# Kernel tuning notes

Measured on AMD Instinct MI355X. Metric: run time of the kernel, lower is better.

Reference implementation:

```python
import jax, jax.numpy as jnp
import numpy as np

N, H, TAU = 320, 160, 257
EPS = 1e-5
LAG_CUT = 33  # output keeps lags 33..TAU-1


def setup_inputs() -> dict:
    key = jax.random.key(0)
    x = jax.random.normal(key, (32, 160000), dtype=jnp.float32)
    return {"x": x}


def reference(x):
    B, S = x.shape
    # prepare_input: pad with H zeros, frame with unfold(N, H)
    xp = jnp.concatenate([x, jnp.zeros((B, H), x.dtype)], axis=1)
    Fn = (S + H - N) // H + 1  # num_frames (static)
    idx = jnp.arange(Fn)[:, None] * H + jnp.arange(N)[None, :]
    frames = xp[:, idx]                      # (B, Fn, N)

    # extract: torch rolls the FLATTENED frames tensor (B, Fn*N) by -tau.
    # x_tau frame f is the window xf[f*N + tau : f*N + tau + N] (circular over Fn*N).
    xf = frames.reshape(B, Fn * N)
    ext_full = jnp.concatenate([xf, xf[:, :TAU - 1]], axis=1)  # circular wrap
    widx = jnp.arange(Fn)[:, None] * N + jnp.arange(N + TAU - 1)[None, :]
    ext = ext_full[:, widx]                  # (B, Fn, N+TAU-1)

    # numerator for all lags at once via grouped 1D cross-correlation
    inp = ext.reshape(1, B * Fn, N + TAU - 1)   # NCW
    ker = frames.reshape(B * Fn, 1, N)          # OIW
    num = jax.lax.conv_general_dilated(
        inp, ker, window_strides=(1,), padding='VALID',
        feature_group_count=B * Fn)             # (1, B*Fn, TAU)
    num = num.reshape(B, Fn, TAU)

    # energies: sum(x*x) per frame, and sliding sum(x_tau*x_tau) via cumsum
    e0 = jnp.sum(frames * frames, axis=-1)      # (B, Fn)
    cs = jnp.concatenate(
        [jnp.zeros((B, Fn, 1), x.dtype), jnp.cumsum(ext * ext, axis=-1)], axis=-1)
    e_tau = cs[..., N:N + TAU] - cs[..., :TAU]  # (B, Fn, TAU)

    xcorr = 2.0 * num / (e0[..., None] + e_tau + EPS)
    return xcorr[:, :, LAG_CUT:]
```

## Files before the change

kernel.cpp:

```cpp
#include <hip/hip_runtime.h>


typedef _Float16 f16;
typedef _Float16 h8 __attribute__((ext_vector_type(8)));
typedef _Float16 h4 __attribute__((ext_vector_type(4)));
typedef float    f4 __attribute__((ext_vector_type(4)));

#define S_LEN 160000
#define FN    1000
#define NF    8
#define BLOCK 256
#define USZ   1536

#define ZPAD_OFF 0
#define SE_OFF   16
#define SO_OFF   3152
#define TH_OFF   6288
#define TO_OFF   6864
#define BRE_OFF  7440
#define BRO_OFF  7952
#define CSG_OFF  8464
#define CST_OFF  14672
#define TOT_OFF  15712
#define SMEM_SZ  16752

__global__ __launch_bounds__(BLOCK)
void xcorr_kernel(const float* __restrict__ x, float* __restrict__ out) {
    __shared__ __align__(16) unsigned char smem[SMEM_SZ];
    f16*      zpad = (f16*)(smem + ZPAD_OFF);
    f16*      s_h  = (f16*)(smem + SE_OFF);
    unsigned* sOd  = (unsigned*)(smem + SO_OFF);
    f16*      T_h  = (f16*)(smem + TH_OFF);
    unsigned* TOd  = (unsigned*)(smem + TO_OFF);
    f16*      brE  = (f16*)(smem + BRE_OFF);
    unsigned* brOd = (unsigned*)(smem + BRO_OFF);
    float*    csg  = (float*)(smem + CSG_OFF);
    float*    csT  = (float*)(smem + CST_OFF);
    float*    tot  = (float*)(smem + TOT_OFF);

    const int tid   = threadIdx.x;
    const int b     = blockIdx.y;
    const int fbase = blockIdx.x * NF;
    const long bOff = (long)b * S_LEN;
    const int gbase = fbase * 160;
    const bool lastBlk = (fbase + NF >= FN);

    for (int i = 4*tid; i < USZ; i += 4*BLOCK) {
        const int gx = gbase + i;
        float v0, v1, v2, v3;
        if (gx + 3 < S_LEN) {
            const float4 v = *(const float4*)&x[bOff + gx];
            v0 = v.x; v1 = v.y; v2 = v.z; v3 = v.w;
        } else {
            v0 = (gx+0 < S_LEN) ? x[bOff+gx+0] : 0.f;
            v1 = (gx+1 < S_LEN) ? x[bOff+gx+1] : 0.f;
            v2 = (gx+2 < S_LEN) ? x[bOff+gx+2] : 0.f;
            v3 = (gx+3 < S_LEN) ? x[bOff+gx+3] : 0.f;
        }
        h4 hv; hv[0]=(f16)v0; hv[1]=(f16)v1; hv[2]=(f16)v2; hv[3]=(f16)v3;
        *(h4*)&s_h[i] = hv;
        f4 sq; sq[0]=v0*v0; sq[1]=v1*v1; sq[2]=v2*v2; sq[3]=v3*v3;
        *(f4*)&csg[i] = sq;
    }
    if (tid < 8) {
        h4 z; z[0]=(f16)0.f; z[1]=(f16)0.f; z[2]=(f16)0.f; z[3]=(f16)0.f;
        *(h4*)&s_h[1536 + 4*tid] = z;
    }
    if (tid < 16) csg[1536 + tid] = 0.f;
    if (tid == 0) { uint4 z; z.x=z.y=z.z=z.w=0u; *(uint4*)(smem + ZPAD_OFF) = z; }
    if (lastBlk) {
        for (int j = tid; j < 288; j += BLOCK) {
            const float tv = (j < 256) ? x[bOff + j] : 0.f;
            T_h[j] = (f16)tv;
            if (j < 260) csT[j] = tv * tv;
        }
    }
    __syncthreads();

    {
        const unsigned* sEd = (const unsigned*)s_h;
        for (int idx = tid; idx < 196; idx += BLOCK) {
            uint4 lo4;
            if (idx) lo4 = *(const uint4*)(sEd + 4*idx - 4);
            else     { lo4.x=lo4.y=lo4.z=0u; lo4.w=0u; }
            const uint4 hi4 = *(const uint4*)(sEd + 4*idx);
            uint4 o;
            o.x = __builtin_amdgcn_alignbit(hi4.x, lo4.w, 16);
            o.y = __builtin_amdgcn_alignbit(hi4.y, hi4.x, 16);
            o.z = __builtin_amdgcn_alignbit(hi4.z, hi4.y, 16);
            o.w = __builtin_amdgcn_alignbit(hi4.w, hi4.z, 16);
            *(uint4*)(sOd + 4*idx) = o;
        }
        if (lastBlk) {
            const unsigned* THd = (const unsigned*)T_h;
            for (int idx = tid; idx < 36; idx += BLOCK) {
                uint4 lo4;
                if (idx) lo4 = *(const uint4*)(THd + 4*idx - 4);
                else     { lo4.x=lo4.y=lo4.z=0u; lo4.w=0u; }
                const uint4 hi4 = *(const uint4*)(THd + 4*idx);
                uint4 o;
                o.x = __builtin_amdgcn_alignbit(hi4.x, lo4.w, 16);
                o.y = __builtin_amdgcn_alignbit(hi4.y, hi4.x, 16);
                o.z = __builtin_amdgcn_alignbit(hi4.z, hi4.y, 16);
                o.w = __builtin_amdgcn_alignbit(hi4.w, hi4.z, 16);
                *(uint4*)(TOd + 4*idx) = o;
            }
        }
        {
            const int fi = tid >> 5, j = tid & 31;
            const int t = 304 + j;
            const bool lastF = lastBlk && (fbase + fi == FN-1);
            f16 v;
            if (t < 320)      v = s_h[160*fi + t];
            else if (lastF)   v = T_h[t - 320];
            else              v = s_h[160*fi + t - 160];
            brE[32*fi + j] = v;
        }
        if (tid < NF*16) {
            const int fi = tid >> 4, j = tid & 15;
            const int tl = 303 + 2*j, th = 304 + 2*j;
            const bool lastF = lastBlk && (fbase + fi == FN-1);
            const f16 lo = (tl < 320) ? s_h[160*fi + tl]
                          : (lastF ? T_h[tl-320] : s_h[160*fi + tl - 160]);
            const f16 hi = (th < 320) ? s_h[160*fi + th]
                          : (lastF ? T_h[th-320] : s_h[160*fi + th - 160]);
            union { struct { f16 a, c; } h; unsigned u; } pk;
            pk.h.a = lo; pk.h.c = hi;
            brOd[16*fi + j] = pk.u;
        }
    }
    float p[7]; float mytot = 0.f;
    {
        const int t0 = 7*tid;
#pragma unroll
        for (int e = 0; e < 7; ++e) {
            const float r = (t0+e < 1552) ? csg[t0+e] : 0.f;
            p[e] = mytot;
            mytot += r;
        }
        tot[tid] = mytot;
    }
    __syncthreads();

    const int lane = tid & 63;
    const int wv   = tid >> 6;
    {
        const float v = tot[tid];
        float sc = v;
#pragma unroll
        for (int d = 1; d < 64; d <<= 1) {
            const float o = __shfl_up(sc, d);
            sc += (lane >= d) ? o : 0.f;
        }
        tot[tid] = sc - v;
        if (lane == 63) tot[256 + wv] = sc;
        if (lastBlk && wv == 0) {
            float r[5]; float mt = 0.f;
#pragma unroll
            for (int e = 0; e < 5; ++e) {
                const int j = 5*lane + e;
                const float rv = (j < 260) ? csT[j] : 0.f;
                r[e] = mt; mt += rv;
            }
            float sc2 = mt;
#pragma unroll
            for (int d = 1; d < 64; d <<= 1) {
                const float o = __shfl_up(sc2, d);
                sc2 += (lane >= d) ? o : 0.f;
            }
            const float b2 = sc2 - mt;
#pragma unroll
            for (int e = 0; e < 5; ++e) {
                const int j = 5*lane + e;
                if (j < 260) csT[j] = b2 + r[e];
            }
        }
    }
    __syncthreads();

    {
        const float w1 = tot[256], w2 = tot[257], w3 = tot[258];
        const float wbase = ((wv > 0) ? w1 : 0.f) + ((wv > 1) ? w2 : 0.f)
                          + ((wv > 2) ? w3 : 0.f);
        const float base = wbase + tot[tid];
        const int t0 = 7*tid;
#pragma unroll
        for (int e = 0; e < 7; ++e)
            if (t0+e < 1552) csg[t0+e] = base + p[e];
    }
    __syncthreads();

    const int col  = lane & 15;
    const int q    = lane >> 4;
    const int off0 = 8*q - 16*col;
    const int tb0  = 33 + col + 8*q;
    const int pc   = tb0 & 1;
    const unsigned* bbS = pc ? sOd : (const unsigned*)s_h;
    const unsigned* bbT = pc ? TOd : (const unsigned*)T_h;

#pragma unroll 1
    for (int ff = 0; ff < 2; ++ff) {
        const int fi = 2*wv + ff;
        const int f  = fbase + fi;
        const bool isLast = (f == FN-1);
        const f16* frame = s_h + 160*fi;
        const int i0 = (160*fi + tb0 + pc) >> 1;
        const unsigned* pA = bbS + i0;
        const unsigned* pB = isLast ? (bbT + ((tb0 - 320 + pc) >> 1))
                                    : (bbS + (i0 - 80));
        const unsigned* brB = pc ? (brOd + 16*fi) : ((const unsigned*)brE + 16*fi);
        const unsigned* p8 = (tb0 <= 56) ? pA
                           : ((tb0 <= 63) ? (brB + ((tb0 - 48 + pc) >> 1) - 128)
                                          : pB);
        f4 acc = {0.f, 0.f, 0.f, 0.f};
#pragma unroll
        for (int s = 0; s < 17; ++s) {
            const int off = off0 + 32*s;
            const f16* ap = ((unsigned)off <= 312u) ? (frame + off) : zpad;
            const h8 a = *(const h8*)ap;
            const unsigned* bp = (s < 8) ? pA : ((s == 8) ? p8 : pB);
            union { unsigned u[4]; h8 h; } Bf;
            Bf.u[0] = bp[16*s + 0];
            Bf.u[1] = bp[16*s + 1];
            Bf.u[2] = bp[16*s + 2];
            Bf.u[3] = bp[16*s + 3];
            acc = __builtin_amdgcn_mfma_f32_16x16x32_f16(a, Bf.h, acc, 0, 0, 0);
        }
        const int D = 160*fi;
        const float c0   = csg[D];
        const float c160 = csg[D+160];
        const float c320 = csg[D+320];
        const float e0   = c320 - c0;
        float* op = &out[(long)(b*FN + f) * 224];
#pragma unroll
        for (int v = 0; v < 4; ++v) {
            const int t1 = 4*q + v;
            if (t1 <= 13) {
                const int tau = 33 + 16*t1 + col;
                const float et = isLast
                    ? (c320 - csg[D+tau] + csT[tau])
                    : (c320 - csg[D+tau] - c160 + csg[D+160+tau]);
                const float den = e0 + et + 1e-5f;
                op[tau - 33] = 2.f * acc[v] * __builtin_amdgcn_rcpf(den);
            }
        }
    }
}

extern "C" void kernel_launch(void* const* d_in, const int* in_sizes, int n_in,
                              void* d_out, int out_size, void* d_ws, size_t ws_size,
                              hipStream_t stream) {
    const float* x = (const float*)d_in[0];
    float* out = (float*)d_out;
    dim3 grid(FN / NF, 32);
    dim3 block(BLOCK);
    hipLaunchKernelGGL(xcorr_kernel, grid, block, 0, stream, x, out);
}
```

Measured before the change: 91.00 us.

## Use one wave per frame with 512 threads and prebuilt padded A-operand buffers

```diff
diff --git a/kernel.cpp b/kernel.cpp
--- a/kernel.cpp
+++ b/kernel.cpp
@@ -9,34 +9,35 @@
 #define S_LEN 160000
 #define FN    1000
 #define NF    8
-#define BLOCK 256
+#define BLOCK 512
 #define USZ   1536
 
-#define ZPAD_OFF 0
-#define SE_OFF   16
-#define SO_OFF   3152
-#define TH_OFF   6288
-#define TO_OFF   6864
-#define BRE_OFF  7440
-#define BRO_OFF  7952
-#define CSG_OFF  8464
-#define CST_OFF  14672
-#define TOT_OFF  15712
-#define SMEM_SZ  16752
+#define SH_OFF   0
+#define SO_OFF   3136
+#define TH_OFF   6272
+#define TO_OFF   6848
+#define BRO_OFF  7424
+#define FP0_OFF  7936
+#define FP1_OFF  13824
+#define CSG_OFF  19712
+#define CST_OFF  27904
+#define TOT_OFF  28944
+#define SMEM_SZ  31024
 
 __global__ __launch_bounds__(BLOCK)
 void xcorr_kernel(const float* __restrict__ x, float* __restrict__ out) {
     __shared__ __align__(16) unsigned char smem[SMEM_SZ];
-    f16*      zpad = (f16*)(smem + ZPAD_OFF);
-    f16*      s_h  = (f16*)(smem + SE_OFF);
+    f16*      s_h  = (f16*)(smem + SH_OFF);
     unsigned* sOd  = (unsigned*)(smem + SO_OFF);
     f16*      T_h  = (f16*)(smem + TH_OFF);
     unsigned* TOd  = (unsigned*)(smem + TO_OFF);
-    f16*      brE  = (f16*)(smem + BRE_OFF);
     unsigned* brOd = (unsigned*)(smem + BRO_OFF);
+    unsigned* fp0  = (unsigned*)(smem + FP0_OFF);
+    unsigned* fp1  = (unsigned*)(smem + FP1_OFF);
     float*    csg  = (float*)(smem + CSG_OFF);
     float*    csT  = (float*)(smem + CST_OFF);
     float*    tot  = (float*)(smem + TOT_OFF);
+    f4*       csg4 = (f4*)csg;
 
     const int tid   = threadIdx.x;
     const int b     = blockIdx.y;
@@ -45,45 +46,47 @@
     const int gbase = fbase * 160;
     const bool lastBlk = (fbase + NF >= FN);
 
-    for (int i = 4*tid; i < USZ; i += 4*BLOCK) {
-        const int gx = gbase + i;
-        float v0, v1, v2, v3;
-        if (gx + 3 < S_LEN) {
-            const float4 v = *(const float4*)&x[bOff + gx];
-            v0 = v.x; v1 = v.y; v2 = v.z; v3 = v.w;
+    {
+        const int i = 4 * tid;
+        if (i < USZ) {
+            const int gx = gbase + i;
+            float v0, v1, v2, v3;
+            if (gx + 3 < S_LEN) {
+                const float4 v = *(const float4*)&x[bOff + gx];
+                v0 = v.x; v1 = v.y; v2 = v.z; v3 = v.w;
+            } else {
+                v0 = (gx+0 < S_LEN) ? x[bOff+gx+0] : 0.f;
+                v1 = (gx+1 < S_LEN) ? x[bOff+gx+1] : 0.f;
+                v2 = (gx+2 < S_LEN) ? x[bOff+gx+2] : 0.f;
+                v3 = (gx+3 < S_LEN) ? x[bOff+gx+3] : 0.f;
+            }
+            h4 hv; hv[0]=(f16)v0; hv[1]=(f16)v1; hv[2]=(f16)v2; hv[3]=(f16)v3;
+            *(h4*)&s_h[i] = hv;
+            f4 sq; sq[0]=v0*v0; sq[1]=v1*v1; sq[2]=v2*v2; sq[3]=v3*v3;
+            csg4[tid] = sq;
         } else {
-            v0 = (gx+0 < S_LEN) ? x[bOff+gx+0] : 0.f;
-            v1 = (gx+1 < S_LEN) ? x[bOff+gx+1] : 0.f;
-            v2 = (gx+2 < S_LEN) ? x[bOff+gx+2] : 0.f;
-            v3 = (gx+3 < S_LEN) ? x[bOff+gx+3] : 0.f;
-        }
-        h4 hv; hv[0]=(f16)v0; hv[1]=(f16)v1; hv[2]=(f16)v2; hv[3]=(f16)v3;
-        *(h4*)&s_h[i] = hv;
-        f4 sq; sq[0]=v0*v0; sq[1]=v1*v1; sq[2]=v2*v2; sq[3]=v3*v3;
-        *(f4*)&csg[i] = sq;
+            f4 z; z[0]=z[1]=z[2]=z[3]=0.f;
+            csg4[tid] = z;
+        }
     }
     if (tid < 8) {
         h4 z; z[0]=(f16)0.f; z[1]=(f16)0.f; z[2]=(f16)0.f; z[3]=(f16)0.f;
         *(h4*)&s_h[1536 + 4*tid] = z;
     }
-    if (tid < 16) csg[1536 + tid] = 0.f;
-    if (tid == 0) { uint4 z; z.x=z.y=z.z=z.w=0u; *(uint4*)(smem + ZPAD_OFF) = z; }
-    if (lastBlk) {
-        for (int j = tid; j < 288; j += BLOCK) {
-            const float tv = (j < 256) ? x[bOff + j] : 0.f;
-            T_h[j] = (f16)tv;
-            if (j < 260) csT[j] = tv * tv;
-        }
-    }
-    __syncthreads();
-
-    {
-        const unsigned* sEd = (const unsigned*)s_h;
+    if (lastBlk && tid < 288) {
+        const float tv = (tid < 256) ? x[bOff + tid] : 0.f;
+        T_h[tid] = (f16)tv;
+        if (tid < 260) csT[tid] = tv * tv;
+    }
+    __syncthreads();
+
+    {
+        const unsigned* sd = (const unsigned*)s_h;
         for (int idx = tid; idx < 196; idx += BLOCK) {
             uint4 lo4;
-            if (idx) lo4 = *(const uint4*)(sEd + 4*idx - 4);
+            if (idx) lo4 = *(const uint4*)(sd + 4*idx - 4);
             else     { lo4.x=lo4.y=lo4.z=0u; lo4.w=0u; }
-            const uint4 hi4 = *(const uint4*)(sEd + 4*idx);
+            const uint4 hi4 = *(const uint4*)(sd + 4*idx);
             uint4 o;
             o.x = __builtin_amdgcn_alignbit(hi4.x, lo4.w, 16);
             o.y = __builtin_amdgcn_alignbit(hi4.y, hi4.x, 16);
@@ -92,12 +95,12 @@
             *(uint4*)(sOd + 4*idx) = o;
         }
         if (lastBlk) {
-            const unsigned* THd = (const unsigned*)T_h;
+            const unsigned* Td = (const unsigned*)T_h;
             for (int idx = tid; idx < 36; idx += BLOCK) {
                 uint4 lo4;
-                if (idx) lo4 = *(const uint4*)(THd + 4*idx - 4);
+                if (idx) lo4 = *(const uint4*)(Td + 4*idx - 4);
                 else     { lo4.x=lo4.y=lo4.z=0u; lo4.w=0u; }
-                const uint4 hi4 = *(const uint4*)(THd + 4*idx);
+                const uint4 hi4 = *(const uint4*)(Td + 4*idx);
                 uint4 o;
                 o.x = __builtin_amdgcn_alignbit(hi4.x, lo4.w, 16);
                 o.y = __builtin_amdgcn_alignbit(hi4.y, hi4.x, 16);
@@ -106,20 +109,34 @@
                 *(uint4*)(TOd + 4*idx) = o;
             }
         }
-        {
-            const int fi = tid >> 5, j = tid & 31;
-            const int t = 304 + j;
+        const uint4* sh4 = (const uint4*)s_h;
+        for (int idx = tid; idx < 368; idx += BLOCK) {
+            const int fi = idx / 46;
+            const int c  = idx - 46*fi;
+            uint4 o0, o1;
+            if (c < 2 || c > 42) {
+                o0.x=o0.y=o0.z=0u; o0.w=0u; o1 = o0;
+            } else if (c == 42) {
+                o0.x=o0.y=o0.z=0u; o0.w=0u;
+                const unsigned prev = sd[80*fi + 159];
+                o1.x = __builtin_amdgcn_alignbit(0u, prev, 16);
+                o1.y = 0u; o1.z = 0u; o1.w = 0u;
+            } else {
+                const uint4 A = sh4[20*fi + c - 2];
+                o0 = A;
+                const unsigned prev = (c == 2) ? 0u : sd[80*fi + 4*c - 9];
+                o1.x = __builtin_amdgcn_alignbit(A.x, prev, 16);
+                o1.y = __builtin_amdgcn_alignbit(A.y, A.x, 16);
+                o1.z = __builtin_amdgcn_alignbit(A.z, A.y, 16);
+                o1.w = __builtin_amdgcn_alignbit(A.w, A.z, 16);
+            }
+            *(uint4*)(fp0 + 184*fi + 4*c) = o0;
+            *(uint4*)(fp1 + 184*fi + 4*c) = o1;
+        }
+        if (tid < 128) {
+            const int fi = tid >> 4, j = tid & 15;
             const bool lastF = lastBlk && (fbase + fi == FN-1);
-            f16 v;
-            if (t < 320)      v = s_h[160*fi + t];
-            else if (lastF)   v = T_h[t - 320];
-            else              v = s_h[160*fi + t - 160];
-            brE[32*fi + j] = v;
-        }
-        if (tid < NF*16) {
-            const int fi = tid >> 4, j = tid & 15;
             const int tl = 303 + 2*j, th = 304 + 2*j;
-            const bool lastF = lastBlk && (fbase + fi == FN-1);
             const f16 lo = (tl < 320) ? s_h[160*fi + tl]
                           : (lastF ? T_h[tl-320] : s_h[160*fi + tl - 160]);
             const f16 hi = (th < 320) ? s_h[160*fi + th]
@@ -129,15 +146,14 @@
             brOd[16*fi + j] = pk.u;
         }
     }
-    float p[7]; float mytot = 0.f;
-    {
-        const int t0 = 7*tid;
-#pragma unroll
-        for (int e = 0; e < 7; ++e) {
-            const float r = (t0+e < 1552) ? csg[t0+e] : 0.f;
-            p[e] = mytot;
-            mytot += r;
-        }
+    float p[4]; float mytot;
+    {
+        const f4 v = csg4[tid];
+        p[0] = 0.f;
+        p[1] = v[0];
+        p[2] = v[0] + v[1];
+        p[3] = p[2] + v[2];
+        mytot = p[3] + v[3];
         tot[tid] = mytot;
     }
     __syncthreads();
@@ -153,7 +169,7 @@
             sc += (lane >= d) ? o : 0.f;
         }
         tot[tid] = sc - v;
-        if (lane == 63) tot[256 + wv] = sc;
+        if (lane == 63) tot[512 + wv] = sc;
         if (lastBlk && wv == 0) {
             float r[5]; float mt = 0.f;
 #pragma unroll
@@ -179,53 +195,48 @@
     __syncthreads();
 
     {
-        const float w1 = tot[256], w2 = tot[257], w3 = tot[258];
-        const float wbase = ((wv > 0) ? w1 : 0.f) + ((wv > 1) ? w2 : 0.f)
-                          + ((wv > 2) ? w3 : 0.f);
+        float wbase = 0.f;
+#pragma unroll
+        for (int w2 = 0; w2 < 7; ++w2)
+            wbase += (wv > w2) ? tot[512 + w2] : 0.f;
         const float base = wbase + tot[tid];
-        const int t0 = 7*tid;
-#pragma unroll
-        for (int e = 0; e < 7; ++e)
-            if (t0+e < 1552) csg[t0+e] = base + p[e];
-    }
-    __syncthreads();
-
-    const int col  = lane & 15;
-    const int q    = lane >> 4;
-    const int off0 = 8*q - 16*col;
-    const int tb0  = 33 + col + 8*q;
-    const int pc   = tb0 & 1;
-    const unsigned* bbS = pc ? sOd : (const unsigned*)s_h;
-    const unsigned* bbT = pc ? TOd : (const unsigned*)T_h;
-
-#pragma unroll 1
-    for (int ff = 0; ff < 2; ++ff) {
-        const int fi = 2*wv + ff;
-        const int f  = fbase + fi;
-        const bool isLast = (f == FN-1);
-        const f16* frame = s_h + 160*fi;
-        const int i0 = (160*fi + tb0 + pc) >> 1;
-        const unsigned* pA = bbS + i0;
-        const unsigned* pB = isLast ? (bbT + ((tb0 - 320 + pc) >> 1))
-                                    : (bbS + (i0 - 80));
-        const unsigned* brB = pc ? (brOd + 16*fi) : ((const unsigned*)brE + 16*fi);
-        const unsigned* p8 = (tb0 <= 56) ? pA
-                           : ((tb0 <= 63) ? (brB + ((tb0 - 48 + pc) >> 1) - 128)
-                                          : pB);
-        f4 acc = {0.f, 0.f, 0.f, 0.f};
-#pragma unroll
-        for (int s = 0; s < 17; ++s) {
-            const int off = off0 + 32*s;
-            const f16* ap = ((unsigned)off <= 312u) ? (frame + off) : zpad;
-            const h8 a = *(const h8*)ap;
-            const unsigned* bp = (s < 8) ? pA : ((s == 8) ? p8 : pB);
-            union { unsigned u[4]; h8 h; } Bf;
-            Bf.u[0] = bp[16*s + 0];
-            Bf.u[1] = bp[16*s + 1];
-            Bf.u[2] = bp[16*s + 2];
-            Bf.u[3] = bp[16*s + 3];
-            acc = __builtin_amdgcn_mfma_f32_16x16x32_f16(a, Bf.h, acc, 0, 0, 0);
-        }
+        f4 o; o[0]=base+p[0]; o[1]=base+p[1]; o[2]=base+p[2]; o[3]=base+p[3];
+        csg4[tid] = o;
+    }
+    __syncthreads();
+
+    const int col = lane & 15;
+    const int q   = lane >> 4;
+    const int fi  = wv;
+    const int f   = fbase + fi;
+    const bool isLast = (f == FN-1);
+
+    const unsigned* ap = (col & 1)
+        ? (fp1 + 184*fi + ((8*q - col + 17) >> 1))
+        : (fp0 + 184*fi + ((8*q - col + 16) >> 1));
+    const int tb0 = 33 + 14*col + 8*q;
+    const int j0  = (tb0 + 1) >> 1;
+    const unsigned* pA  = sOd + 80*fi + j0;
+    const unsigned* pB  = isLast ? (TOd + j0 - 160) : (pA - 80);
+    const int sA   = (312 - tb0) >> 5;
+    const int sStr = (319 - tb0) >> 5;
+    const unsigned* pbr = brOd + 16*fi + ((tb0 + 32*sStr - 303) >> 1) - 16*sStr;
+
+    f4 acc = {0.f, 0.f, 0.f, 0.f};
+#pragma unroll
+    for (int s = 0; s < 11; ++s) {
+        const uint2 a0 = *(const uint2*)(ap + 16*s);
+        const uint2 a1 = *(const uint2*)(ap + 16*s + 2);
+        const unsigned* bp = (s <= sA) ? pA : ((s == sStr) ? pbr : pB);
+        const uint2 b0 = *(const uint2*)(bp + 16*s);
+        const uint2 b1 = *(const uint2*)(bp + 16*s + 2);
+        union { unsigned u[4]; h8 h; } Af, Bf;
+        Af.u[0] = a0.x; Af.u[1] = a0.y; Af.u[2] = a1.x; Af.u[3] = a1.y;
+        Bf.u[0] = b0.x; Bf.u[1] = b0.y; Bf.u[2] = b1.x; Bf.u[3] = b1.y;
+        acc = __builtin_amdgcn_mfma_f32_16x16x32_f16(Af.h, Bf.h, acc, 0, 0, 0);
+    }
+
+    {
         const int D = 160*fi;
         const float c0   = csg[D];
         const float c160 = csg[D+160];
@@ -236,12 +247,12 @@
         for (int v = 0; v < 4; ++v) {
             const int t1 = 4*q + v;
             if (t1 <= 13) {
-                const int tau = 33 + 16*t1 + col;
+                const int tau = 33 + t1 + 14*col;
                 const float et = isLast
                     ? (c320 - csg[D+tau] + csT[tau])
                     : (c320 - csg[D+tau] - c160 + csg[D+160+tau]);
                 const float den = e0 + et + 1e-5f;
-                op[tau - 33] = 2.f * acc[v] * __builtin_amdgcn_rcpf(den);
+                op[t1 + 14*col] = 2.f * acc[v] * __builtin_amdgcn_rcpf(den);
             }
         }
     }
```

Measured after the change: 230.9 us. 154% more time.

## Share B-fragment loads across the two frames each wave processes

Applied to the files above, without the earlier changes.

```diff
diff --git a/kernel.cpp b/kernel.cpp
--- a/kernel.cpp
+++ b/kernel.cpp
@@ -92,12 +92,12 @@
             *(uint4*)(sOd + 4*idx) = o;
         }
         if (lastBlk) {
-            const unsigned* THd = (const unsigned*)T_h;
+            const unsigned* Td = (const unsigned*)T_h;
             for (int idx = tid; idx < 36; idx += BLOCK) {
                 uint4 lo4;
-                if (idx) lo4 = *(const uint4*)(THd + 4*idx - 4);
+                if (idx) lo4 = *(const uint4*)(Td + 4*idx - 4);
                 else     { lo4.x=lo4.y=lo4.z=0u; lo4.w=0u; }
-                const uint4 hi4 = *(const uint4*)(THd + 4*idx);
+                const uint4 hi4 = *(const uint4*)(Td + 4*idx);
                 uint4 o;
                 o.x = __builtin_amdgcn_alignbit(hi4.x, lo4.w, 16);
                 o.y = __builtin_amdgcn_alignbit(hi4.y, hi4.x, 16);
@@ -198,50 +198,93 @@
     const unsigned* bbS = pc ? sOd : (const unsigned*)s_h;
     const unsigned* bbT = pc ? TOd : (const unsigned*)T_h;
 
-#pragma unroll 1
-    for (int ff = 0; ff < 2; ++ff) {
-        const int fi = 2*wv + ff;
-        const int f  = fbase + fi;
-        const bool isLast = (f == FN-1);
-        const f16* frame = s_h + 160*fi;
-        const int i0 = (160*fi + tb0 + pc) >> 1;
-        const unsigned* pA = bbS + i0;
-        const unsigned* pB = isLast ? (bbT + ((tb0 - 320 + pc) >> 1))
-                                    : (bbS + (i0 - 80));
-        const unsigned* brB = pc ? (brOd + 16*fi) : ((const unsigned*)brE + 16*fi);
-        const unsigned* p8 = (tb0 <= 56) ? pA
-                           : ((tb0 <= 63) ? (brB + ((tb0 - 48 + pc) >> 1) - 128)
-                                          : pB);
-        f4 acc = {0.f, 0.f, 0.f, 0.f};
-#pragma unroll
-        for (int s = 0; s < 17; ++s) {
-            const int off = off0 + 32*s;
-            const f16* ap = ((unsigned)off <= 312u) ? (frame + off) : zpad;
-            const h8 a = *(const h8*)ap;
-            const unsigned* bp = (s < 8) ? pA : ((s == 8) ? p8 : pB);
-            union { unsigned u[4]; h8 h; } Bf;
-            Bf.u[0] = bp[16*s + 0];
-            Bf.u[1] = bp[16*s + 1];
-            Bf.u[2] = bp[16*s + 2];
-            Bf.u[3] = bp[16*s + 3];
-            acc = __builtin_amdgcn_mfma_f32_16x16x32_f16(a, Bf.h, acc, 0, 0, 0);
-        }
-        const int D = 160*fi;
+    const int g = 2*wv, h = g + 1;
+    const int fg = fbase + g, fh = fbase + h;
+    const bool isLastH = (fh == FN-1);
+    const f16* frg = s_h + 160*g;
+    const f16* frh = s_h + 160*h;
+    const int j0 = (tb0 + pc) >> 1;
+    const unsigned* pS  = bbS + 80*g + j0;
+    const unsigned* pTB = bbT + ((tb0 - 320 + pc) >> 1);
+    const unsigned* brBg = pc ? (brOd + 16*g) : ((const unsigned*)brE + 16*g);
+    const unsigned* brBh = pc ? (brOd + 16*h) : ((const unsigned*)brE + 16*h);
+    const unsigned* pBh  = isLastH ? pTB : pS;
+    const unsigned* p8g  = (tb0 <= 56) ? pS
+                         : ((tb0 <= 63) ? (brBg + ((tb0 - 48 + pc) >> 1) - 128)
+                                        : (pS - 80));
+    const unsigned* p8h  = (tb0 <= 56) ? (pS + 80)
+                         : ((tb0 <= 63) ? (brBh + ((tb0 - 48 + pc) >> 1) - 128)
+                                        : pBh);
+
+    auto ALOAD = [&](const f16* frm, int s_) -> h8 {
+        const int off_ = off0 + 32*s_;
+        const f16* ap_ = ((unsigned)off_ <= 312u) ? (frm + off_) : zpad;
+        return *(const h8*)ap_;
+    };
+    auto BLOAD = [&](const unsigned* bp, int o) -> h8 {
+        union { unsigned u[4]; h8 hh; } B_;
+        B_.u[0] = bp[o+0]; B_.u[1] = bp[o+1];
+        B_.u[2] = bp[o+2]; B_.u[3] = bp[o+3];
+        return B_.hh;
+    };
+
+    f4 accg = {0.f, 0.f, 0.f, 0.f};
+    f4 acch = {0.f, 0.f, 0.f, 0.f};
+#pragma unroll
+    for (int u = 0; u < 17; ++u) {
+        const h8 F = BLOAD(pS, 16*u);
+        if (u <= 7)
+            accg = __builtin_amdgcn_mfma_f32_16x16x32_f16(ALOAD(frg, u),   F, accg, 0, 0, 0);
+        if (u >= 4 && u <= 11)
+            accg = __builtin_amdgcn_mfma_f32_16x16x32_f16(ALOAD(frg, u+5), F, accg, 0, 0, 0);
+        if (u >= 5 && u <= 12)
+            acch = __builtin_amdgcn_mfma_f32_16x16x32_f16(ALOAD(frh, u-5), F, acch, 0, 0, 0);
+        if (u >= 9 && !isLastH)
+            acch = __builtin_amdgcn_mfma_f32_16x16x32_f16(ALOAD(frh, u),   F, acch, 0, 0, 0);
+    }
+    accg = __builtin_amdgcn_mfma_f32_16x16x32_f16(ALOAD(frg, 8), BLOAD(p8g, 128), accg, 0, 0, 0);
+    acch = __builtin_amdgcn_mfma_f32_16x16x32_f16(ALOAD(frh, 8), BLOAD(p8h, 128), acch, 0, 0, 0);
+    if (isLastH) {
+#pragma unroll
+        for (int s = 9; s < 17; ++s)
+            acch = __builtin_amdgcn_mfma_f32_16x16x32_f16(ALOAD(frh, s), BLOAD(pTB, 16*s), acch, 0, 0, 0);
+    }
+
+    {
+        const int D = 160*g;
         const float c0   = csg[D];
         const float c160 = csg[D+160];
         const float c320 = csg[D+320];
         const float e0   = c320 - c0;
-        float* op = &out[(long)(b*FN + f) * 224];
+        float* op = &out[(long)(b*FN + fg) * 224];
 #pragma unroll
         for (int v = 0; v < 4; ++v) {
             const int t1 = 4*q + v;
             if (t1 <= 13) {
                 const int tau = 33 + 16*t1 + col;
-                const float et = isLast
+                const float et = c320 - csg[D+tau] - c160 + csg[D+160+tau];
+                const float den = e0 + et + 1e-5f;
+                op[tau - 33] = 2.f * accg[v] * __builtin_amdgcn_rcpf(den);
+            }
+        }
+    }
+    {
+        const int D = 160*h;
+        const float c0   = csg[D];
+        const float c160 = csg[D+160];
+        const float c320 = csg[D+320];
+        const float e0   = c320 - c0;
+        float* op = &out[(long)(b*FN + fh) * 224];
+#pragma unroll
+        for (int v = 0; v < 4; ++v) {
+            const int t1 = 4*q + v;
+            if (t1 <= 13) {
+                const int tau = 33 + 16*t1 + col;
+                const float et = isLastH
                     ? (c320 - csg[D+tau] + csT[tau])
                     : (c320 - csg[D+tau] - c160 + csg[D+160+tau]);
                 const float den = e0 + et + 1e-5f;
-                op[tau - 33] = 2.f * acc[v] * __builtin_amdgcn_rcpf(den);
+                op[tau - 33] = 2.f * acch[v] * __builtin_amdgcn_rcpf(den);
             }
         }
     }
```

After: 86.34 us. -5.1%, faster.
